# Kernel optimization log

Measured on AMD Instinct MI355X. Metric: run time of the kernel, lower is better.

Reference implementation:

```python
import jax, jax.numpy as jnp
import numpy as np

EPS = 1e-8  # torch F.cosine_similarity denominator clamp
MARGIN = 0.1  # default M in forward signature


def setup_inputs() -> dict:
    key = jax.random.key(0)
    k1, k2 = jax.random.split(key)
    N, B, D = 4096, 1, 1024
    wsi = jax.random.normal(k1, (N, B, D), dtype=jnp.float32)
    omic = jax.random.normal(k2, (N, B, D), dtype=jnp.float32)
    return {"wsi_embeddings": wsi, "omic_embeddings": omic}


def reference(wsi_embeddings, omic_embeddings):
    # [N, B=1, D] -> [N, D]
    W = wsi_embeddings[:, 0, :]
    O = omic_embeddings[:, 0, :]
    nw = jnp.linalg.norm(W, axis=-1)  # [N]
    no = jnp.linalg.norm(O, axis=-1)  # [N]
    # Full pairwise cosine similarity: S[i, j] = cos(wsi_i, omic_j)
    S = (W @ O.T) / jnp.maximum(nw[:, None] * no[None, :], EPS)  # [N, N]
    d = jnp.diagonal(S)  # cos(wsi_i, omic_i), the "self" similarity
    # off-diagonal hinge: relu(M - cos_ij + cos_ii); diagonal: 1 - cos_ii
    off = jax.nn.relu(MARGIN - S + d[:, None])
    eye = jnp.eye(S.shape[0], dtype=bool)
    L = jnp.where(eye, 1.0 - S, off)
    return jnp.mean(L)
```

## Files before the change

kernel.cpp:

```cpp
#include <hip/hip_runtime.h>
#include <stdint.h>

#define N 4096
#define D 1024
#define MARGIN 0.1f
#define BM 64
#define BN 128
#define BKB 128
#define SCALE_ONE 0x7F

typedef __attribute__((ext_vector_type(4))) float f32x4;
typedef __attribute__((ext_vector_type(8))) int i32x8;

__global__ __launch_bounds__(256) void prep_kernel(
    const float* __restrict__ W, const float* __restrict__ O,
    uint8_t* __restrict__ Wn, uint8_t* __restrict__ On,
    float* __restrict__ dvec, float* __restrict__ out) {
  const int wv = threadIdx.x >> 6, ln = threadIdx.x & 63;
  const int row = blockIdx.x * 4 + wv;
  if (blockIdx.x == 0 && threadIdx.x == 0) *out = 0.0f;
  const float4* Wr = (const float4*)(W + (size_t)row * D);
  const float4* Or = (const float4*)(O + (size_t)row * D);
  float4 w[4], o[4];
  float sw = 0.f, so = 0.f, sd = 0.f;
  #pragma unroll
  for (int c = 0; c < 4; ++c) {
    w[c] = Wr[ln + c * 64];
    o[c] = Or[ln + c * 64];
    sw += w[c].x * w[c].x + w[c].y * w[c].y + w[c].z * w[c].z + w[c].w * w[c].w;
    so += o[c].x * o[c].x + o[c].y * o[c].y + o[c].z * o[c].z + o[c].w * o[c].w;
    sd += w[c].x * o[c].x + w[c].y * o[c].y + w[c].z * o[c].z + w[c].w * o[c].w;
  }
  #pragma unroll
  for (int off = 1; off < 64; off <<= 1) {
    sw += __shfl_xor(sw, off, 64);
    so += __shfl_xor(so, off, 64);
    sd += __shfl_xor(sd, off, 64);
  }
  const float inw = 1.0f / sqrtf(sw);
  const float ino = 1.0f / sqrtf(so);
  if (ln == 0) dvec[row] = sd * inw * ino;
  int* Wo = (int*)(Wn + (size_t)row * D);
  int* Oo = (int*)(On + (size_t)row * D);
  #pragma unroll
  for (int c = 0; c < 4; ++c) {
    int pw = __builtin_amdgcn_cvt_pk_fp8_f32(w[c].x * inw, w[c].y * inw, 0, false);
    pw = __builtin_amdgcn_cvt_pk_fp8_f32(w[c].z * inw, w[c].w * inw, pw, true);
    int po = __builtin_amdgcn_cvt_pk_fp8_f32(o[c].x * ino, o[c].y * ino, 0, false);
    po = __builtin_amdgcn_cvt_pk_fp8_f32(o[c].z * ino, o[c].w * ino, po, true);
    Wo[ln + c * 64] = pw;
    Oo[ln + c * 64] = po;
  }
}

__global__ __launch_bounds__(256) void gemm_loss_kernel(
    const uint8_t* __restrict__ Wn, const uint8_t* __restrict__ On,
    const float* __restrict__ dvec, float* __restrict__ out) {
  __shared__ __align__(16) uint8_t ldsA[BM * BKB];
  __shared__ __align__(16) uint8_t ldsB[BN * BKB];
  const int bx = blockIdx.x, by = blockIdx.y;
  const int t = threadIdx.x;
  const int wv = t >> 6, ln = t & 63;
  const int wm = wv >> 1, wn = wv & 1;
  const int lrow = ln & 15;
  const int quad = ln >> 4;
  const int l7 = lrow & 7;

  f32x4 acc[2][4] = {};

  const int gA = t;
  const int rA0 = gA >> 3, giA0 = gA & 7;
  const int rA1 = (gA + 256) >> 3, giA1 = (gA + 256) & 7;
  const uint8_t* Ag = Wn + (size_t)(by * BM) * D;
  const uint8_t* Bg = On + (size_t)(bx * BN) * D;

  const int goff0 = (((2 * quad) ^ l7) << 4);
  const int goff1 = (((2 * quad + 1) ^ l7) << 4);
  const uint8_t* aBase0 = ldsA + (wm * 32 + lrow) * BKB;
  const uint8_t* aBase1 = aBase0 + 16 * BKB;
  const uint8_t* bBase = ldsB + (wn * 64 + lrow) * BKB;

  #pragma unroll 1
  for (int kt = 0; kt < D / BKB; ++kt) {
    const size_t kb = (size_t)kt * BKB;
    __builtin_amdgcn_global_load_lds(
        (const __attribute__((address_space(1))) void*)(Ag + (size_t)rA0 * D + kb + ((giA0 ^ (rA0 & 7)) << 4)),
        (__attribute__((address_space(3))) void*)(ldsA + gA * 16), 16, 0, 0);
    __builtin_amdgcn_global_load_lds(
        (const __attribute__((address_space(1))) void*)(Ag + (size_t)rA1 * D + kb + ((giA1 ^ (rA1 & 7)) << 4)),
        (__attribute__((address_space(3))) void*)(ldsA + (gA + 256) * 16), 16, 0, 0);
    #pragma unroll
    for (int c = 0; c < 4; ++c) {
      const int g = c * 256 + t;
      const int r = g >> 3;
      const int gi = g & 7;
      __builtin_amdgcn_global_load_lds(
          (const __attribute__((address_space(1))) void*)(Bg + (size_t)r * D + kb + ((gi ^ (r & 7)) << 4)),
          (__attribute__((address_space(3))) void*)(ldsB + g * 16), 16, 0, 0);
    }
    __syncthreads();

    i32x8 aF[2];
    {
      const int4 lo0 = *(const int4*)(aBase0 + goff0);
      const int4 hi0 = *(const int4*)(aBase0 + goff1);
      aF[0] = (i32x8){lo0.x, lo0.y, lo0.z, lo0.w, hi0.x, hi0.y, hi0.z, hi0.w};
      const int4 lo1 = *(const int4*)(aBase1 + goff0);
      const int4 hi1 = *(const int4*)(aBase1 + goff1);
      aF[1] = (i32x8){lo1.x, lo1.y, lo1.z, lo1.w, hi1.x, hi1.y, hi1.z, hi1.w};
    }
    #pragma unroll
    for (int ni = 0; ni < 4; ++ni) {
      const uint8_t* base = bBase + ni * 16 * BKB;
      const int4 lo = *(const int4*)(base + goff0);
      const int4 hi = *(const int4*)(base + goff1);
      const i32x8 bF = (i32x8){lo.x, lo.y, lo.z, lo.w, hi.x, hi.y, hi.z, hi.w};
      acc[0][ni] = __builtin_amdgcn_mfma_scale_f32_16x16x128_f8f6f4(
          aF[0], bF, acc[0][ni], 0, 0, 0, SCALE_ONE, 0, SCALE_ONE);
      acc[1][ni] = __builtin_amdgcn_mfma_scale_f32_16x16x128_f8f6f4(
          aF[1], bF, acc[1][ni], 0, 0, 0, SCALE_ONE, 0, SCALE_ONE);
    }
    __syncthreads();
  }

  float lsum = 0.0f;
  #pragma unroll
  for (int mi = 0; mi < 2; ++mi) {
    const int gibase = by * BM + wm * 32 + mi * 16 + quad * 4;
    #pragma unroll
    for (int r = 0; r < 4; ++r) {
      const int gi = gibase + r;
      const float di = dvec[gi];
      #pragma unroll
      for (int ni = 0; ni < 4; ++ni) {
        const int gj = bx * BN + wn * 64 + ni * 16 + lrow;
        const float s = acc[mi][ni][r];
        lsum += (gi == gj) ? (1.0f - s) : fmaxf(MARGIN - s + di, 0.0f);
      }
    }
  }
  #pragma unroll
  for (int off = 32; off; off >>= 1) lsum += __shfl_down(lsum, off, 64);
  __shared__ float bsum[4];
  if (ln == 0) bsum[wv] = lsum;
  __syncthreads();
  if (t == 0) {
    const float tot = (bsum[0] + bsum[1] + bsum[2] + bsum[3]) *
                      (1.0f / ((float)N * (float)N));
    atomicAdd(out, tot);
  }
}

extern "C" void kernel_launch(void* const* d_in, const int* in_sizes, int n_in,
                              void* d_out, int out_size, void* d_ws, size_t ws_size,
                              hipStream_t stream) {
  const float* W = (const float*)d_in[0];
  const float* O = (const float*)d_in[1];
  uint8_t* Wn = (uint8_t*)d_ws;
  uint8_t* On = Wn + (size_t)N * D;
  float* dvec = (float*)(On + (size_t)N * D);
  float* out = (float*)d_out;

  prep_kernel<<<N / 4, 256, 0, stream>>>(W, O, Wn, On, dvec, out);
  dim3 grid(N / BN, N / BM);
  gemm_loss_kernel<<<grid, 256, 0, stream>>>(Wn, On, dvec, out);
}
```

Before: 112.5 us.

## Double-buffer LDS tiles and prefetch next K-slice during MFMA compute

Doubles the LDS buffers for A and B and issues the async global-to-LDS loads for the next K tile before computing on the current one. Also drops the trailing barrier, so there is one barrier per iteration. The aim is to hide global load latency behind the MFMA work. In exchange, LDS use doubles to 48KB per block, which can lower occupancy, and the scheme depends on the barrier draining the outstanding async loads.

```diff
diff --git a/kernel.cpp b/kernel.cpp
--- a/kernel.cpp
+++ b/kernel.cpp
@@ -8,6 +8,8 @@
 #define BN 128
 #define BKB 128
 #define SCALE_ONE 0x7F
+#define ASZ (BM * BKB)
+#define BSZ (BN * BKB)
 
 typedef __attribute__((ext_vector_type(4))) float f32x4;
 typedef __attribute__((ext_vector_type(8))) int i32x8;
@@ -56,8 +58,8 @@
 __global__ __launch_bounds__(256) void gemm_loss_kernel(
     const uint8_t* __restrict__ Wn, const uint8_t* __restrict__ On,
     const float* __restrict__ dvec, float* __restrict__ out) {
-  __shared__ __align__(16) uint8_t ldsA[BM * BKB];
-  __shared__ __align__(16) uint8_t ldsB[BN * BKB];
+  __shared__ __align__(16) uint8_t ldsA[2 * ASZ];
+  __shared__ __align__(16) uint8_t ldsB[2 * BSZ];
   const int bx = blockIdx.x, by = blockIdx.y;
   const int t = threadIdx.x;
   const int wv = t >> 6, ln = t & 63;
@@ -68,50 +70,74 @@
 
   f32x4 acc[2][4] = {};
 
-  const int gA = t;
-  const int rA0 = gA >> 3, giA0 = gA & 7;
-  const int rA1 = (gA + 256) >> 3, giA1 = (gA + 256) & 7;
   const uint8_t* Ag = Wn + (size_t)(by * BM) * D;
   const uint8_t* Bg = On + (size_t)(bx * BN) * D;
 
+  const int rA0 = t >> 3,           cA0 = (((t & 7) ^ (rA0 & 7)) << 4);
+  const int rA1 = (t + 256) >> 3,   cA1 = ((((t + 256) & 7) ^ (rA1 & 7)) << 4);
+
   const int goff0 = (((2 * quad) ^ l7) << 4);
   const int goff1 = (((2 * quad + 1) ^ l7) << 4);
-  const uint8_t* aBase0 = ldsA + (wm * 32 + lrow) * BKB;
-  const uint8_t* aBase1 = aBase0 + 16 * BKB;
-  const uint8_t* bBase = ldsB + (wn * 64 + lrow) * BKB;
+  const int aRow0 = (wm * 32 + lrow) * BKB;
+  const int bRow = (wn * 64 + lrow) * BKB;
 
-  #pragma unroll 1
-  for (int kt = 0; kt < D / BKB; ++kt) {
-    const size_t kb = (size_t)kt * BKB;
+  {
     __builtin_amdgcn_global_load_lds(
-        (const __attribute__((address_space(1))) void*)(Ag + (size_t)rA0 * D + kb + ((giA0 ^ (rA0 & 7)) << 4)),
-        (__attribute__((address_space(3))) void*)(ldsA + gA * 16), 16, 0, 0);
+        (const __attribute__((address_space(1))) void*)(Ag + (size_t)rA0 * D + cA0),
+        (__attribute__((address_space(3))) void*)(ldsA + t * 16), 16, 0, 0);
     __builtin_amdgcn_global_load_lds(
-        (const __attribute__((address_space(1))) void*)(Ag + (size_t)rA1 * D + kb + ((giA1 ^ (rA1 & 7)) << 4)),
-        (__attribute__((address_space(3))) void*)(ldsA + (gA + 256) * 16), 16, 0, 0);
+        (const __attribute__((address_space(1))) void*)(Ag + (size_t)rA1 * D + cA1),
+        (__attribute__((address_space(3))) void*)(ldsA + (t + 256) * 16), 16, 0, 0);
     #pragma unroll
     for (int c = 0; c < 4; ++c) {
       const int g = c * 256 + t;
       const int r = g >> 3;
-      const int gi = g & 7;
+      const int col = (((g & 7) ^ (r & 7)) << 4);
       __builtin_amdgcn_global_load_lds(
-          (const __attribute__((address_space(1))) void*)(Bg + (size_t)r * D + kb + ((gi ^ (r & 7)) << 4)),
+          (const __attribute__((address_space(1))) void*)(Bg + (size_t)r * D + col),
           (__attribute__((address_space(3))) void*)(ldsB + g * 16), 16, 0, 0);
     }
+  }
+
+  #pragma unroll 1
+  for (int kt = 0; kt < D / BKB; ++kt) {
+    const int cur = kt & 1;
     __syncthreads();
 
+    if (kt < D / BKB - 1) {
+      const size_t kb = (size_t)(kt + 1) * BKB;
+      const int nxt = cur ^ 1;
+      __builtin_amdgcn_global_load_lds(
+          (const __attribute__((address_space(1))) void*)(Ag + (size_t)rA0 * D + kb + cA0),
+          (__attribute__((address_space(3))) void*)(ldsA + nxt * ASZ + t * 16), 16, 0, 0);
+      __builtin_amdgcn_global_load_lds(
+          (const __attribute__((address_space(1))) void*)(Ag + (size_t)rA1 * D + kb + cA1),
+          (__attribute__((address_space(3))) void*)(ldsA + nxt * ASZ + (t + 256) * 16), 16, 0, 0);
+      #pragma unroll
+      for (int c = 0; c < 4; ++c) {
+        const int g = c * 256 + t;
+        const int r = g >> 3;
+        const int col = (((g & 7) ^ (r & 7)) << 4);
+        __builtin_amdgcn_global_load_lds(
+            (const __attribute__((address_space(1))) void*)(Bg + (size_t)r * D + kb + col),
+            (__attribute__((address_space(3))) void*)(ldsB + nxt * BSZ + g * 16), 16, 0, 0);
+      }
+    }
+
+    const uint8_t* aB = ldsA + cur * ASZ + aRow0;
+    const uint8_t* bB = ldsB + cur * BSZ + bRow;
     i32x8 aF[2];
     {
-      const int4 lo0 = *(const int4*)(aBase0 + goff0);
-      const int4 hi0 = *(const int4*)(aBase0 + goff1);
+      const int4 lo0 = *(const int4*)(aB + goff0);
+      const int4 hi0 = *(const int4*)(aB + goff1);
       aF[0] = (i32x8){lo0.x, lo0.y, lo0.z, lo0.w, hi0.x, hi0.y, hi0.z, hi0.w};
-      const int4 lo1 = *(const int4*)(aBase1 + goff0);
-      const int4 hi1 = *(const int4*)(aBase1 + goff1);
+      const int4 lo1 = *(const int4*)(aB + 16 * BKB + goff0);
+      const int4 hi1 = *(const int4*)(aB + 16 * BKB + goff1);
       aF[1] = (i32x8){lo1.x, lo1.y, lo1.z, lo1.w, hi1.x, hi1.y, hi1.z, hi1.w};
     }
     #pragma unroll
     for (int ni = 0; ni < 4; ++ni) {
-      const uint8_t* base = bBase + ni * 16 * BKB;
+      const uint8_t* base = bB + ni * 16 * BKB;
       const int4 lo = *(const int4*)(base + goff0);
       const int4 hi = *(const int4*)(base + goff1);
       const i32x8 bF = (i32x8){lo.x, lo.y, lo.z, lo.w, hi.x, hi.y, hi.z, hi.w};
@@ -120,7 +146,6 @@
       acc[1][ni] = __builtin_amdgcn_mfma_scale_f32_16x16x128_f8f6f4(
           aF[1], bF, acc[1][ni], 0, 0, 0, SCALE_ONE, 0, SCALE_ONE);
     }
-    __syncthreads();
   }
 
   float lsum = 0.0f;
```

Result: no change. 113.7 us (+1.1%).
